# Optimization experiments

Measured on AMD Instinct MI355X. Metric: run time of the kernel, lower is better.

The kernel has to match this reference:

```python
import jax, jax.numpy as jnp
import numpy as np

B, S, D, H = 2, 2048, 1024, 16
HD = D // H  # head dim = 64


def setup_inputs() -> dict:
    key = jax.random.key(0)
    ks = jax.random.split(key, 9)
    s_in = 1.0 / np.sqrt(D)
    s_out = 1.0 / np.sqrt(HD)
    return {
        "x": jax.random.normal(ks[0], (B, S, D), jnp.float32),
        "Wq": jax.random.normal(ks[1], (D, H, HD), jnp.float32) * s_in,
        "bq": jnp.zeros((H, HD), jnp.float32),
        "Wk": jax.random.normal(ks[2], (D, H, HD), jnp.float32) * s_in,
        "bk": jnp.zeros((H, HD), jnp.float32),
        "Wv": jax.random.normal(ks[3], (D, H, HD), jnp.float32) * s_in,
        "bv": jnp.zeros((H, HD), jnp.float32),
        "Wo": jax.random.normal(ks[4], (H, HD, D), jnp.float32) * s_out,
        "bo": jnp.zeros((D,), jnp.float32),
    }


def reference(x, Wq, bq, Wk, bk, Wv, bv, Wo, bo):
    # QKV projections: [B,S,D] -> [B,S,H,HD]
    q = jnp.einsum("bsd,dhk->bshk", x, Wq) + bq
    k = jnp.einsum("bsd,dhk->bshk", x, Wk) + bk
    v = jnp.einsum("bsd,dhk->bshk", x, Wv) + bv

    # scaled dot-product attention (matches nnx.dot_product_attention)
    scale = jnp.asarray(1.0 / np.sqrt(HD), q.dtype)
    scores = jnp.einsum("bqhk,bshk->bhqs", q * scale, k)  # [B,H,S,S]
    attn = jax.nn.softmax(scores, axis=-1)
    y = jnp.einsum("bhqs,bshk->bqhk", attn, v)  # [B,S,H,HD]

    # exclusive post-processing: subtract projection onto L2-normalized v
    eps = jnp.asarray(1e-12, v.dtype)
    v_norm = v * jax.lax.rsqrt(jnp.sum(jnp.square(v), axis=-1, keepdims=True) + eps)
    y = y - jnp.sum(y * v_norm, axis=-1, keepdims=True) * v_norm

    # output projection: [B,S,H,HD] -> [B,S,D]
    out = jnp.einsum("bshk,hkd->bsd", y, Wo) + bo
    return out  # dropout is identity (deterministic=True)
```

## Files before the change

### kernel.cpp

```cpp
#include <hip/hip_runtime.h>

#define BB 2
#define SS 2048
#define DD 1024
#define HH 16
#define HDD 64

typedef __attribute__((ext_vector_type(4))) float f32x4;
typedef __attribute__((ext_vector_type(8))) short short8;
typedef __attribute__((ext_vector_type(4))) short short4v;

__device__ __forceinline__ short f2bf(float f) {
    union { float f; unsigned u; } a; a.f = f;
    unsigned r = a.u + 0x7fffu + ((a.u >> 16) & 1u);
    return (short)(r >> 16);
}
__device__ __forceinline__ float bf2f(short s) {
    union { unsigned u; float f; } a; a.u = ((unsigned)(unsigned short)s) << 16;
    return a.f;
}
__device__ __forceinline__ float fast_exp2(float x) {
    float r;
    asm("v_exp_f32 %0, %1\n\ts_nop 0" : "=v"(r) : "v"(x));
    return r;
}
__device__ __forceinline__ unsigned cvt_pk_bf16(float lo, float hi) {
    unsigned r;
    asm("v_cvt_pk_bf16_f32 %0, %1, %2" : "=v"(r) : "v"(lo), "v"(hi));
    return r;
}
__device__ __forceinline__ float fmax3(float a, float b, float c) {
    float r;
    asm("v_max3_f32 %0, %1, %2, %3" : "=v"(r) : "v"(a), "v"(b), "v"(c));
    return r;
}

#define GLD16(gp, lp) __builtin_amdgcn_global_load_lds( \
    (const __attribute__((address_space(1))) void*)(gp), \
    (__attribute__((address_space(3))) void*)(lp), 16, 0, 0)

__global__ __launch_bounds__(256) void conv_x(const float* __restrict__ src,
                                              short* __restrict__ dst)
{
    const int i = (blockIdx.x * 256 + threadIdx.x) * 8;
    f32x4 a = *(const f32x4*)(src + i);
    f32x4 b = *(const f32x4*)(src + i + 4);
    short8 o;
    #pragma unroll
    for (int j = 0; j < 4; j++) { o[j] = f2bf(a[j]); o[j + 4] = f2bf(b[j]); }
    *(short8*)(dst + i) = o;
}

__global__ __launch_bounds__(256) void conv_w4(
    const float* __restrict__ Wq, const float* __restrict__ Wk,
    const float* __restrict__ Wv, const float* __restrict__ Wo,
    short* __restrict__ Wt, short* __restrict__ Wot, float qscale)
{
    __shared__ float t[64][65];
    const int z = blockIdx.z;
    const float* src = (z == 0) ? Wq : (z == 1) ? Wk : (z == 2) ? Wv : Wo;
    short* dst = (z < 3) ? (Wt + (size_t)z * 1048576) : Wot;
    const float scale = (z == 0) ? qscale : 1.f;

    const int tid = threadIdx.x;
    const int c = tid & 63, rg = tid >> 6;
    const int bi = blockIdx.x * 64, bj = blockIdx.y * 64;
    #pragma unroll
    for (int i = 0; i < 16; i++)
        t[rg * 16 + i][c] = src[(size_t)(bi + rg * 16 + i) * 1024 + bj + c];
    __syncthreads();
    #pragma unroll
    for (int i = 0; i < 16; i++)
        dst[(size_t)(bj + rg * 16 + i) * 1024 + bi + c] = f2bf(scale * t[c][rg * 16 + i]);
}

__global__ __launch_bounds__(256) void conv_bias(const float* __restrict__ bq,
                                                 const float* __restrict__ bk,
                                                 const float* __restrict__ bv,
                                                 float* __restrict__ bcat, float qscale)
{
    const int i = blockIdx.x * 256 + threadIdx.x;
    float v = (i < 1024) ? bq[i] * qscale : (i < 2048 ? bk[i - 1024] : bv[i - 2048]);
    bcat[i] = v;
}

template<int KIND>
__global__ __launch_bounds__(256, 2) void gemm_mfma(
    const short* __restrict__ A, const short* __restrict__ Bt,
    const float* __restrict__ bias,
    short* __restrict__ oQ, short* __restrict__ oK, short* __restrict__ oV,
    float* __restrict__ oF)
{
    __shared__ short lds[32768];
    const int tid = threadIdx.x;
    const int lane = tid & 63;
    const int ln15 = lane & 15, g = lane >> 4;
    const int wid = tid >> 6;
    const int wm = wid >> 1, wn = wid & 1;
    const int bm = blockIdx.x * 128;
    const int bn = blockIdx.y * 128;
    const bool vpath = (KIND == 0) && (blockIdx.y >= 16);

    f32x4 acc[4][4];
    #pragma unroll
    for (int i = 0; i < 4; i++)
        #pragma unroll
        for (int j = 0; j < 4; j++) acc[i][j] = (f32x4){0.f, 0.f, 0.f, 0.f};

    const int sr = lane >> 3, cs = lane & 7;
    const int sc8 = (cs ^ sr) << 3;
    const int rb = wid * 8;

    auto stage = [&](int buf, int k0) {
        #pragma unroll
        for (int j = 0; j < 4; j++) {
            const int r = rb + j * 32 + sr;
            GLD16(A + (size_t)(bm + r) * 1024 + k0 + sc8,
                  &lds[buf * 16384 + (rb + j * 32) * 64]);
            GLD16(Bt + (size_t)(bn + r) * 1024 + k0 + sc8,
                  &lds[buf * 16384 + 8192 + (rb + j * 32) * 64]);
        }
    };

    stage(0, 0);
    asm volatile("s_waitcnt vmcnt(0)" ::: "memory");
    __builtin_amdgcn_s_barrier();

    for (int t = 0; t < 16; ++t) {
        const int cur = t & 1;
        if (t < 15) stage(cur ^ 1, (t + 1) * 64);
        const char* base = (const char*)lds + cur * 32768;

        #pragma unroll
        for (int kk = 0; kk < 2; kk++) {
            short8 af[4], bf[4];
            #pragma unroll
            for (int f = 0; f < 4; f++) {
                const int ra = wm * 64 + f * 16 + ln15;
                af[f] = *(const short8*)(base + ra * 128 +
                                         ((((kk << 2) | g) ^ (ra & 7)) << 4));
                const int rbv = wn * 64 + f * 16 + ln15;
                bf[f] = *(const short8*)(base + 16384 + rbv * 128 +
                                         ((((kk << 2) | g) ^ (rbv & 7)) << 4));
            }
            __builtin_amdgcn_s_setprio(1);
            if (!vpath) {
                #pragma unroll
                for (int fm = 0; fm < 4; fm++)
                    #pragma unroll
                    for (int fn = 0; fn < 4; fn++)
                        acc[fm][fn] = __builtin_amdgcn_mfma_f32_16x16x32_bf16(
                            bf[fn], af[fm], acc[fm][fn], 0, 0, 0);
            } else {
                #pragma unroll
                for (int fm = 0; fm < 4; fm++)
                    #pragma unroll
                    for (int fn = 0; fn < 4; fn++)
                        acc[fm][fn] = __builtin_amdgcn_mfma_f32_16x16x32_bf16(
                            af[fm], bf[fn], acc[fm][fn], 0, 0, 0);
            }
            __builtin_amdgcn_s_setprio(0);
        }
        asm volatile("s_waitcnt vmcnt(0) lgkmcnt(0)" ::: "memory");
        __builtin_amdgcn_s_barrier();
    }

    const int n_base = bn + wn * 64;

    if constexpr (KIND == 1) {
        #pragma unroll
        for (int fn = 0; fn < 4; fn++) {
            const int n0 = n_base + fn * 16 + 4 * g;
            const f32x4 b4 = *(const f32x4*)(bias + n0);
            #pragma unroll
            for (int fm = 0; fm < 4; fm++) {
                const int t = bm + wm * 64 + fm * 16 + ln15;
                f32x4 o = acc[fm][fn] + b4;
                *(f32x4*)(oF + (size_t)t * 1024 + n0) = o;
            }
        }
    } else if (!vpath) {
        short* dst = (n_base < 1024) ? oQ : oK;
        #pragma unroll
        for (int fn = 0; fn < 4; fn++) {
            const int n0 = n_base + fn * 16 + 4 * g;
            const f32x4 b4 = *(const f32x4*)(bias + n0);
            const int nl = n0 & 1023;
            const int h = nl >> 6, d = nl & 63;
            #pragma unroll
            for (int fm = 0; fm < 4; fm++) {
                const int t = bm + wm * 64 + fm * 16 + ln15;
                const int b = t >> 11, s = t & 2047;
                short4v pk = { f2bf(acc[fm][fn][0] + b4[0]), f2bf(acc[fm][fn][1] + b4[1]),
                               f2bf(acc[fm][fn][2] + b4[2]), f2bf(acc[fm][fn][3] + b4[3]) };
                *(short4v*)(dst + ((size_t)(b * HH + h) * SS + s) * HDD + d) = pk;
            }
        }
    } else {
        #pragma unroll
        for (int fn = 0; fn < 4; fn++) {
            const int nf = n_base + fn * 16 + ln15;
            const float bb = bias[nf];
            const int nl = nf - 2048;
            const int h = nl >> 6, d = nl & 63;
            #pragma unroll
            for (int fm = 0; fm < 4; fm++) {
                const int t0 = bm + wm * 64 + fm * 16 + 4 * g;
                const int b = t0 >> 11;
                const int sb = (t0 & 2047) & ~63;
                const int pos = g * 16 + (fm & 1) * 4 + ((fm >> 1) & 1) * 8;
                short4v pk = { f2bf(acc[fm][fn][0] + bb), f2bf(acc[fm][fn][1] + bb),
                               f2bf(acc[fm][fn][2] + bb), f2bf(acc[fm][fn][3] + bb) };
                *(short4v*)(oV + ((size_t)(b * HH + h) * HDD + d) * SS + sb + pos) = pk;
            }
        }
    }
}

__global__ __launch_bounds__(256, 2) void attn_mfma_kernel(
    const short* __restrict__ Qh, const short* __restrict__ Kh,
    const short* __restrict__ Vt, short* __restrict__ yb)
{
    __shared__ short lds[16384];

    const int lane = threadIdx.x & 63;
    const int wid  = threadIdx.x >> 6;
    const int ln15 = lane & 15;
    const int g    = lane >> 4;

    const int bid  = ((int)blockIdx.x & 7) * 64 + ((int)blockIdx.x >> 3);
    const int bh   = bid >> 4;
    const int qB   = (bid & 15) * 128;
    const int qW   = qB + wid * 32;

    const short* qbase = Qh + (size_t)bh * SS * HDD;
    const short* kbase = Kh + (size_t)bh * SS * HDD;
    const short* vtb   = Vt + (size_t)bh * HDD * SS;

    short8 qf[2][2];
    #pragma unroll
    for (int qg = 0; qg < 2; qg++)
        #pragma unroll
        for (int c = 0; c < 2; c++)
            qf[qg][c] = *(const short8*)(qbase +
                (size_t)(qW + qg * 16 + ln15) * HDD + c * 32 + g * 8);

    const short8 ones = { 0x3f80, 0x3f80, 0x3f80, 0x3f80,
                          0x3f80, 0x3f80, 0x3f80, 0x3f80 };

    const int sr = lane >> 3;
    const int cs = lane & 7;
    const int sc8 = (cs ^ sr) << 3;

    auto stage = [&](int b, int s0) {
        #pragma unroll
        for (int j = 0; j < 2; j++) {
            const int rr = wid * 16 + j * 8 + sr;
            GLD16(kbase + (size_t)(s0 + rr) * HDD + sc8,
                  &lds[b * 8192 + (wid * 16 + j * 8) * 64]);
            GLD16(vtb + (size_t)rr * SS + s0 + sc8,
                  &lds[b * 8192 + 4096 + (wid * 16 + j * 8) * 64]);
        }
    };

    f32x4 o[2][4], ol[2];
    #pragma unroll
    for (int qg = 0; qg < 2; qg++) {
        ol[qg] = (f32x4){0.f, 0.f, 0.f, 0.f};
        #pragma unroll
        for (int c = 0; c < 4; c++) o[qg][c] = (f32x4){0.f, 0.f, 0.f, 0.f};
    }
    float m[2] = { -1e30f, -1e30f };

    stage(0, 0);
    asm volatile("s_waitcnt vmcnt(0)" ::: "memory");
    __builtin_amdgcn_s_barrier();

    for (int t = 0; t < SS / 64; ++t) {
        const int cur = t & 1;
        if (t < SS / 64 - 1) stage(cur ^ 1, (t + 1) * 64);

        const char* kb = (const char*)lds + cur * 16384;
        short8 kf[4][2];
        #pragma unroll
        for (int kg = 0; kg < 4; kg++) {
            const int rk = kg * 16 + ln15;
            #pragma unroll
            for (int c = 0; c < 2; c++)
                kf[kg][c] = *(const short8*)(kb + rk * 128 +
                                             (((c * 4 + g) ^ (rk & 7)) << 4));
        }
        const f32x4 z = {0.f, 0.f, 0.f, 0.f};
        f32x4 s[4][2];
        __builtin_amdgcn_s_setprio(1);
        #pragma unroll
        for (int kg = 0; kg < 4; kg++)
            #pragma unroll
            for (int qg = 0; qg < 2; qg++) {
                s[kg][qg] = __builtin_amdgcn_mfma_f32_16x16x32_bf16(
                    kf[kg][0], qf[qg][0], z, 0, 0, 0);
                s[kg][qg] = __builtin_amdgcn_mfma_f32_16x16x32_bf16(
                    kf[kg][1], qf[qg][1], s[kg][qg], 0, 0, 0);
            }
        __builtin_amdgcn_s_setprio(0);

        float pm[2];
        #pragma unroll
        for (int qg = 0; qg < 2; qg++) {
            const float t0 = fmax3(s[0][qg][0], s[0][qg][1], s[0][qg][2]);
            const float t1 = fmax3(s[0][qg][3], s[1][qg][0], s[1][qg][1]);
            const float t2 = fmax3(s[1][qg][2], s[1][qg][3], s[2][qg][0]);
            const float t3 = fmax3(s[2][qg][1], s[2][qg][2], s[2][qg][3]);
            const float t4 = fmax3(s[3][qg][0], s[3][qg][1], s[3][qg][2]);
            pm[qg] = fmaxf(fmax3(t0, t1, t2), fmax3(t3, t4, s[3][qg][3]));
        }
        if (__any((pm[0] > m[0] + 8.f) || (pm[1] > m[1] + 8.f))) {
            #pragma unroll
            for (int qg = 0; qg < 2; qg++) {
                float pmw = fmaxf(pm[qg], __shfl_xor(pm[qg], 16));
                pmw = fmaxf(pmw, __shfl_xor(pmw, 32));
                const float mn = fmaxf(m[qg], pmw);
                const float corr = fast_exp2(m[qg] - mn);
                ol[qg] *= corr;
                #pragma unroll
                for (int c = 0; c < 4; c++) o[qg][c] *= corr;
                m[qg] = mn;
            }
        }

        union { unsigned u[4]; short8 v; } P0[2], P1[2];
        #pragma unroll
        for (int qg = 0; qg < 2; qg++) {
            float p[16];
            #pragma unroll
            for (int kg = 0; kg < 4; kg++)
                #pragma unroll
                for (int r = 0; r < 4; r++)
                    p[kg * 4 + r] = fast_exp2(s[kg][qg][r] - m[qg]);
            P0[qg].u[0] = cvt_pk_bf16(p[0], p[1]);
            P0[qg].u[1] = cvt_pk_bf16(p[2], p[3]);
            P0[qg].u[2] = cvt_pk_bf16(p[4], p[5]);
            P0[qg].u[3] = cvt_pk_bf16(p[6], p[7]);
            P1[qg].u[0] = cvt_pk_bf16(p[8], p[9]);
            P1[qg].u[1] = cvt_pk_bf16(p[10], p[11]);
            P1[qg].u[2] = cvt_pk_bf16(p[12], p[13]);
            P1[qg].u[3] = cvt_pk_bf16(p[14], p[15]);
        }

        const char* vb = kb + 8192;
        __builtin_amdgcn_s_setprio(1);
        #pragma unroll
        for (int c = 0; c < 4; c++) {
            const int rv = c * 16 + ln15;
            const int sw = ln15 & 7;
            short8 vf0 = *(const short8*)(vb + rv * 128 + (((2 * g) ^ sw) << 4));
            short8 vf1 = *(const short8*)(vb + rv * 128 + (((2 * g + 1) ^ sw) << 4));
            #pragma unroll
            for (int qg = 0; qg < 2; qg++) {
                o[qg][c] = __builtin_amdgcn_mfma_f32_16x16x32_bf16(
                    vf0, P0[qg].v, o[qg][c], 0, 0, 0);
                o[qg][c] = __builtin_amdgcn_mfma_f32_16x16x32_bf16(
                    vf1, P1[qg].v, o[qg][c], 0, 0, 0);
            }
        }
        #pragma unroll
        for (int qg = 0; qg < 2; qg++) {
            ol[qg] = __builtin_amdgcn_mfma_f32_16x16x32_bf16(ones, P0[qg].v, ol[qg], 0, 0, 0);
            ol[qg] = __builtin_amdgcn_mfma_f32_16x16x32_bf16(ones, P1[qg].v, ol[qg], 0, 0, 0);
        }
        __builtin_amdgcn_s_setprio(0);

        asm volatile("s_waitcnt vmcnt(0) lgkmcnt(0)" ::: "memory");
        __builtin_amdgcn_s_barrier();
    }

    const int b = bh >> 4, h = bh & 15;
    #pragma unroll
    for (int qg = 0; qg < 2; qg++) {
        const float inv = 1.f / ol[qg][0];
        #pragma unroll
        for (int c = 0; c < 4; c++) o[qg][c] *= inv;

        const int spos = qB + (wid >> 1) * 64 + (ln15 >> 2) * 16 + qg * 4 +
                         (wid & 1) * 8 + (ln15 & 3);
        float v4[4][4];
        float nv = 0.f, dv = 0.f;
        #pragma unroll
        for (int c = 0; c < 4; c++)
            #pragma unroll
            for (int r = 0; r < 4; r++) {
                const float vd = bf2f(vtb[(size_t)(c * 16 + 4 * g + r) * SS + spos]);
                v4[c][r] = vd;
                nv += vd * vd;
                dv += o[qg][c][r] * vd;
            }
        nv += __shfl_xor(nv, 16); nv += __shfl_xor(nv, 32);
        dv += __shfl_xor(dv, 16); dv += __shfl_xor(dv, 32);
        const float tpp = dv / (nv + 1e-12f);

        const int tok = b * SS + qW + qg * 16 + ln15;
        #pragma unroll
        for (int c = 0; c < 4; c++) {
            short4v pk = { f2bf(o[qg][c][0] - v4[c][0] * tpp),
                           f2bf(o[qg][c][1] - v4[c][1] * tpp),
                           f2bf(o[qg][c][2] - v4[c][2] * tpp),
                           f2bf(o[qg][c][3] - v4[c][3] * tpp) };
            *(short4v*)(yb + (size_t)tok * 1024 + h * 64 + c * 16 + 4 * g) = pk;
        }
    }
}

extern "C" void kernel_launch(void* const* d_in, const int* in_sizes, int n_in,
                              void* d_out, int out_size, void* d_ws, size_t ws_size,
                              hipStream_t stream)
{
    const float* x  = (const float*)d_in[0];
    const float* Wq = (const float*)d_in[1];
    const float* bq = (const float*)d_in[2];
    const float* Wk = (const float*)d_in[3];
    const float* bk = (const float*)d_in[4];
    const float* Wv = (const float*)d_in[5];
    const float* bv = (const float*)d_in[6];
    const float* Wo = (const float*)d_in[7];
    const float* bo = (const float*)d_in[8];
    float* out = (float*)d_out;

    char* w = (char*)d_ws;
    short* xb   = (short*)(w);
    short* Wt   = (short*)(w + (8ull << 20));
    short* Wot  = (short*)(w + (14ull << 20));
    float* bcat = (float*)(w + (16ull << 20));
    short* Qh   = (short*)(w + (17ull << 20));
    short* Kh   = (short*)(w + (25ull << 20));
    short* Vt   = (short*)(w + (33ull << 20));
    short* yb   = (short*)(w + (41ull << 20));

    const float qscale = 0.125f * 1.44269504f;
    dim3 blk(256);

    conv_x<<<2048, blk, 0, stream>>>(x, xb);
    conv_w4<<<dim3(16, 16, 4), blk, 0, stream>>>(Wq, Wk, Wv, Wo, Wt, Wot, qscale);
    conv_bias<<<12, blk, 0, stream>>>(bq, bk, bv, bcat, qscale);

    gemm_mfma<0><<<dim3(32, 24), blk, 0, stream>>>(xb, Wt, bcat,
                                                   Qh, Kh, Vt, nullptr);

    attn_mfma_kernel<<<dim3(512), blk, 0, stream>>>(Qh, Kh, Vt, yb);

    gemm_mfma<1><<<dim3(32, 8), blk, 0, stream>>>(yb, Wot, bo,
                                                  nullptr, nullptr, nullptr, out);
}
```

Baseline: 112.8 us.

## Merge conversion kernels, fold bias prep into GEMM, unroll double-buffered loops

The x conversion and the weight-transpose kernels are merged into one launch, and the bias-concatenation kernel is dropped so the QKV GEMM epilogue reads bq/bk/bv directly and applies the q scale itself. Both the GEMM and attention main loops are manually unrolled by two with fixed buffer indices and precomputed LDS and global offsets, which removes per-iteration address arithmetic. The setprio calls around the GEMM MFMAs are removed. Together these cut launch count and scalar/VALU overhead, at the cost of larger code and a changed workspace layout.

```diff
diff --git a/kernel.cpp b/kernel.cpp
--- a/kernel.cpp
+++ b/kernel.cpp
@@ -39,25 +39,30 @@
     (const __attribute__((address_space(1))) void*)(gp), \
     (__attribute__((address_space(3))) void*)(lp), 16, 0, 0)
 
-__global__ __launch_bounds__(256) void conv_x(const float* __restrict__ src,
-                                              short* __restrict__ dst)
-{
-    const int i = (blockIdx.x * 256 + threadIdx.x) * 8;
-    f32x4 a = *(const f32x4*)(src + i);
-    f32x4 b = *(const f32x4*)(src + i + 4);
-    short8 o;
-    #pragma unroll
-    for (int j = 0; j < 4; j++) { o[j] = f2bf(a[j]); o[j + 4] = f2bf(b[j]); }
-    *(short8*)(dst + i) = o;
-}
-
-__global__ __launch_bounds__(256) void conv_w4(
+__global__ __launch_bounds__(256) void conv_all(
+    const float* __restrict__ x,
     const float* __restrict__ Wq, const float* __restrict__ Wk,
     const float* __restrict__ Wv, const float* __restrict__ Wo,
-    short* __restrict__ Wt, short* __restrict__ Wot, float qscale)
+    short* __restrict__ xb, short* __restrict__ Wt, short* __restrict__ Wot,
+    float qscale)
 {
+    const int z = blockIdx.z;
+    if (z == 4) {
+        const int id = blockIdx.x * 16 + blockIdx.y;
+        const size_t base = (size_t)id * 16384 + threadIdx.x * 8;
+        #pragma unroll
+        for (int it = 0; it < 8; ++it) {
+            const size_t i = base + (size_t)it * 2048;
+            f32x4 a = *(const f32x4*)(x + i);
+            f32x4 b = *(const f32x4*)(x + i + 4);
+            short8 o;
+            #pragma unroll
+            for (int j = 0; j < 4; j++) { o[j] = f2bf(a[j]); o[j + 4] = f2bf(b[j]); }
+            *(short8*)(xb + i) = o;
+        }
+        return;
+    }
     __shared__ float t[64][65];
-    const int z = blockIdx.z;
     const float* src = (z == 0) ? Wq : (z == 1) ? Wk : (z == 2) ? Wv : Wo;
     short* dst = (z < 3) ? (Wt + (size_t)z * 1048576) : Wot;
     const float scale = (z == 0) ? qscale : 1.f;
@@ -74,20 +79,11 @@
         dst[(size_t)(bj + rg * 16 + i) * 1024 + bi + c] = f2bf(scale * t[c][rg * 16 + i]);
 }
 
-__global__ __launch_bounds__(256) void conv_bias(const float* __restrict__ bq,
-                                                 const float* __restrict__ bk,
-                                                 const float* __restrict__ bv,
-                                                 float* __restrict__ bcat, float qscale)
-{
-    const int i = blockIdx.x * 256 + threadIdx.x;
-    float v = (i < 1024) ? bq[i] * qscale : (i < 2048 ? bk[i - 1024] : bv[i - 2048]);
-    bcat[i] = v;
-}
-
 template<int KIND>
 __global__ __launch_bounds__(256, 2) void gemm_mfma(
     const short* __restrict__ A, const short* __restrict__ Bt,
-    const float* __restrict__ bias,
+    const float* __restrict__ b0, const float* __restrict__ b1,
+    const float* __restrict__ b2, float qscale,
     short* __restrict__ oQ, short* __restrict__ oK, short* __restrict__ oV,
     float* __restrict__ oF)
 {
@@ -95,6 +91,7 @@
     const int tid = threadIdx.x;
     const int lane = tid & 63;
     const int ln15 = lane & 15, g = lane >> 4;
+    const int swl = ln15 & 7;
     const int wid = tid >> 6;
     const int wm = wid >> 1, wn = wid & 1;
     const int bm = blockIdx.x * 128;
@@ -110,40 +107,42 @@
     const int sr = lane >> 3, cs = lane & 7;
     const int sc8 = (cs ^ sr) << 3;
     const int rb = wid * 8;
-
-    auto stage = [&](int buf, int k0) {
+    const short* Ak = A;
+    const short* Bk = Bt;
+    int aoff[4], boff[4], adst[4];
+    #pragma unroll
+    for (int j = 0; j < 4; j++) {
+        aoff[j] = (bm + rb + j * 32 + sr) * 1024 + sc8;
+        boff[j] = (bn + rb + j * 32 + sr) * 1024 + sc8;
+        adst[j] = (rb + j * 32) * 64;
+    }
+
+    auto stage = [&](int BUF) {
         #pragma unroll
         for (int j = 0; j < 4; j++) {
-            const int r = rb + j * 32 + sr;
-            GLD16(A + (size_t)(bm + r) * 1024 + k0 + sc8,
-                  &lds[buf * 16384 + (rb + j * 32) * 64]);
-            GLD16(Bt + (size_t)(bn + r) * 1024 + k0 + sc8,
-                  &lds[buf * 16384 + 8192 + (rb + j * 32) * 64]);
-        }
+            GLD16(Ak + aoff[j], &lds[BUF * 16384 + adst[j]]);
+            GLD16(Bk + boff[j], &lds[BUF * 16384 + 8192 + adst[j]]);
+        }
+        Ak += 64; Bk += 64;
     };
 
-    stage(0, 0);
-    asm volatile("s_waitcnt vmcnt(0)" ::: "memory");
-    __builtin_amdgcn_s_barrier();
-
-    for (int t = 0; t < 16; ++t) {
-        const int cur = t & 1;
-        if (t < 15) stage(cur ^ 1, (t + 1) * 64);
-        const char* base = (const char*)lds + cur * 32768;
-
+    const char* ldsc = (const char*)lds;
+    int aB[2], bB[2];
+    #pragma unroll
+    for (int kk = 0; kk < 2; kk++) {
+        aB[kk] = (wm * 64 + ln15) * 128 + ((((kk << 2) | g) ^ swl) << 4);
+        bB[kk] = 16384 + (wn * 64 + ln15) * 128 + ((((kk << 2) | g) ^ swl) << 4);
+    }
+
+    auto tilec = [&](int BUF) {
         #pragma unroll
         for (int kk = 0; kk < 2; kk++) {
             short8 af[4], bf[4];
             #pragma unroll
             for (int f = 0; f < 4; f++) {
-                const int ra = wm * 64 + f * 16 + ln15;
-                af[f] = *(const short8*)(base + ra * 128 +
-                                         ((((kk << 2) | g) ^ (ra & 7)) << 4));
-                const int rbv = wn * 64 + f * 16 + ln15;
-                bf[f] = *(const short8*)(base + 16384 + rbv * 128 +
-                                         ((((kk << 2) | g) ^ (rbv & 7)) << 4));
-            }
-            __builtin_amdgcn_s_setprio(1);
+                af[f] = *(const short8*)(ldsc + BUF * 32768 + aB[kk] + f * 2048);
+                bf[f] = *(const short8*)(ldsc + BUF * 32768 + bB[kk] + f * 2048);
+            }
             if (!vpath) {
                 #pragma unroll
                 for (int fm = 0; fm < 4; fm++)
@@ -159,11 +158,29 @@
                         acc[fm][fn] = __builtin_amdgcn_mfma_f32_16x16x32_bf16(
                             af[fm], bf[fn], acc[fm][fn], 0, 0, 0);
             }
-            __builtin_amdgcn_s_setprio(0);
-        }
+        }
+    };
+
+    stage(0);
+    asm volatile("s_waitcnt vmcnt(0)" ::: "memory");
+    __builtin_amdgcn_s_barrier();
+
+    #pragma unroll 1
+    for (int i = 0; i < 7; ++i) {
+        stage(1);
+        tilec(0);
         asm volatile("s_waitcnt vmcnt(0) lgkmcnt(0)" ::: "memory");
         __builtin_amdgcn_s_barrier();
-    }
+        stage(0);
+        tilec(1);
+        asm volatile("s_waitcnt vmcnt(0) lgkmcnt(0)" ::: "memory");
+        __builtin_amdgcn_s_barrier();
+    }
+    stage(1);
+    tilec(0);
+    asm volatile("s_waitcnt vmcnt(0) lgkmcnt(0)" ::: "memory");
+    __builtin_amdgcn_s_barrier();
+    tilec(1);
 
     const int n_base = bn + wn * 64;
 
@@ -171,7 +188,7 @@
         #pragma unroll
         for (int fn = 0; fn < 4; fn++) {
             const int n0 = n_base + fn * 16 + 4 * g;
-            const f32x4 b4 = *(const f32x4*)(bias + n0);
+            const f32x4 b4 = *(const f32x4*)(b0 + n0);
             #pragma unroll
             for (int fm = 0; fm < 4; fm++) {
                 const int t = bm + wm * 64 + fm * 16 + ln15;
@@ -180,12 +197,16 @@
             }
         }
     } else if (!vpath) {
-        short* dst = (n_base < 1024) ? oQ : oK;
+        const bool isq = (n_base < 1024);
+        short* dst = isq ? oQ : oK;
+        const float* bp = isq ? b0 : b1;
+        const float scl = isq ? qscale : 1.f;
         #pragma unroll
         for (int fn = 0; fn < 4; fn++) {
             const int n0 = n_base + fn * 16 + 4 * g;
-            const f32x4 b4 = *(const f32x4*)(bias + n0);
             const int nl = n0 & 1023;
+            f32x4 b4 = *(const f32x4*)(bp + nl);
+            b4 *= scl;
             const int h = nl >> 6, d = nl & 63;
             #pragma unroll
             for (int fm = 0; fm < 4; fm++) {
@@ -200,8 +221,8 @@
         #pragma unroll
         for (int fn = 0; fn < 4; fn++) {
             const int nf = n_base + fn * 16 + ln15;
-            const float bb = bias[nf];
             const int nl = nf - 2048;
+            const float bb = b2[nl];
             const int h = nl >> 6, d = nl & 63;
             #pragma unroll
             for (int fm = 0; fm < 4; fm++) {
@@ -227,6 +248,7 @@
     const int wid  = threadIdx.x >> 6;
     const int ln15 = lane & 15;
     const int g    = lane >> 4;
+    const int swl  = ln15 & 7;
 
     const int bid  = ((int)blockIdx.x & 7) * 64 + ((int)blockIdx.x >> 3);
     const int bh   = bid >> 4;
@@ -251,17 +273,27 @@
     const int sr = lane >> 3;
     const int cs = lane & 7;
     const int sc8 = (cs ^ sr) << 3;
-
-    auto stage = [&](int b, int s0) {
-        #pragma unroll
-        for (int j = 0; j < 2; j++) {
-            const int rr = wid * 16 + j * 8 + sr;
-            GLD16(kbase + (size_t)(s0 + rr) * HDD + sc8,
-                  &lds[b * 8192 + (wid * 16 + j * 8) * 64]);
-            GLD16(vtb + (size_t)rr * SS + s0 + sc8,
-                  &lds[b * 8192 + 4096 + (wid * 16 + j * 8) * 64]);
-        }
+    const int r0 = wid * 16 + sr;
+    const int r1 = wid * 16 + 8 + sr;
+    const short* Kk = kbase;
+    const short* Vk = vtb;
+    const int koff0 = r0 * 64 + sc8, koff1 = r1 * 64 + sc8;
+    const int voff0 = r0 * 2048 + sc8, voff1 = r1 * 2048 + sc8;
+    const int d0 = (wid * 16) * 64, d1 = (wid * 16 + 8) * 64;
+
+    auto stage = [&](int BUF) {
+        GLD16(Kk + koff0, &lds[BUF * 8192 + d0]);
+        GLD16(Kk + koff1, &lds[BUF * 8192 + d1]);
+        GLD16(Vk + voff0, &lds[BUF * 8192 + 4096 + d0]);
+        GLD16(Vk + voff1, &lds[BUF * 8192 + 4096 + d1]);
+        Kk += 4096; Vk += 64;
     };
+
+    const char* ldsc = (const char*)lds;
+    const int kA0 = ln15 * 128 + ((g ^ swl) << 4);
+    const int kA1 = ln15 * 128 + (((4 + g) ^ swl) << 4);
+    const int vA0 = 8192 + ln15 * 128 + (((2 * g) ^ swl) << 4);
+    const int vA1 = 8192 + ln15 * 128 + (((2 * g + 1) ^ swl) << 4);
 
     f32x4 o[2][4], ol[2];
     #pragma unroll
@@ -272,23 +304,12 @@
     }
     float m[2] = { -1e30f, -1e30f };
 
-    stage(0, 0);
-    asm volatile("s_waitcnt vmcnt(0)" ::: "memory");
-    __builtin_amdgcn_s_barrier();
-
-    for (int t = 0; t < SS / 64; ++t) {
-        const int cur = t & 1;
-        if (t < SS / 64 - 1) stage(cur ^ 1, (t + 1) * 64);
-
-        const char* kb = (const char*)lds + cur * 16384;
+    auto tilec = [&](int BUF) {
         short8 kf[4][2];
         #pragma unroll
         for (int kg = 0; kg < 4; kg++) {
-            const int rk = kg * 16 + ln15;
-            #pragma unroll
-            for (int c = 0; c < 2; c++)
-                kf[kg][c] = *(const short8*)(kb + rk * 128 +
-                                             (((c * 4 + g) ^ (rk & 7)) << 4));
+            kf[kg][0] = *(const short8*)(ldsc + BUF * 16384 + kA0 + kg * 2048);
+            kf[kg][1] = *(const short8*)(ldsc + BUF * 16384 + kA1 + kg * 2048);
         }
         const f32x4 z = {0.f, 0.f, 0.f, 0.f};
         f32x4 s[4][2];
@@ -347,14 +368,11 @@
             P1[qg].u[3] = cvt_pk_bf16(p[14], p[15]);
         }
 
-        const char* vb = kb + 8192;
         __builtin_amdgcn_s_setprio(1);
         #pragma unroll
         for (int c = 0; c < 4; c++) {
-            const int rv = c * 16 + ln15;
-            const int sw = ln15 & 7;
-            short8 vf0 = *(const short8*)(vb + rv * 128 + (((2 * g) ^ sw) << 4));
-            short8 vf1 = *(const short8*)(vb + rv * 128 + (((2 * g + 1) ^ sw) << 4));
+            short8 vf0 = *(const short8*)(ldsc + BUF * 16384 + vA0 + c * 2048);
+            short8 vf1 = *(const short8*)(ldsc + BUF * 16384 + vA1 + c * 2048);
             #pragma unroll
             for (int qg = 0; qg < 2; qg++) {
                 o[qg][c] = __builtin_amdgcn_mfma_f32_16x16x32_bf16(
@@ -369,10 +387,28 @@
             ol[qg] = __builtin_amdgcn_mfma_f32_16x16x32_bf16(ones, P1[qg].v, ol[qg], 0, 0, 0);
         }
         __builtin_amdgcn_s_setprio(0);
-
+    };
+
+    stage(0);
+    asm volatile("s_waitcnt vmcnt(0)" ::: "memory");
+    __builtin_amdgcn_s_barrier();
+
+    #pragma unroll 1
+    for (int i = 0; i < 15; ++i) {
+        stage(1);
+        tilec(0);
         asm volatile("s_waitcnt vmcnt(0) lgkmcnt(0)" ::: "memory");
         __builtin_amdgcn_s_barrier();
-    }
+        stage(0);
+        tilec(1);
+        asm volatile("s_waitcnt vmcnt(0) lgkmcnt(0)" ::: "memory");
+        __builtin_amdgcn_s_barrier();
+    }
+    stage(1);
+    tilec(0);
+    asm volatile("s_waitcnt vmcnt(0) lgkmcnt(0)" ::: "memory");
+    __builtin_amdgcn_s_barrier();
+    tilec(1);
 
     const int b = bh >> 4, h = bh & 15;
     #pragma unroll
@@ -429,24 +465,22 @@
     short* xb   = (short*)(w);
     short* Wt   = (short*)(w + (8ull << 20));
     short* Wot  = (short*)(w + (14ull << 20));
-    float* bcat = (float*)(w + (16ull << 20));
-    short* Qh   = (short*)(w + (17ull << 20));
-    short* Kh   = (short*)(w + (25ull << 20));
-    short* Vt   = (short*)(w + (33ull << 20));
-    short* yb   = (short*)(w + (41ull << 20));
+    short* Qh   = (short*)(w + (16ull << 20));
+    short* Kh   = (short*)(w + (24ull << 20));
+    short* Vt   = (short*)(w + (32ull << 20));
+    short* yb   = (short*)(w + (40ull << 20));
 
     const float qscale = 0.125f * 1.44269504f;
     dim3 blk(256);
 
-    conv_x<<<2048, blk, 0, stream>>>(x, xb);
-    conv_w4<<<dim3(16, 16, 4), blk, 0, stream>>>(Wq, Wk, Wv, Wo, Wt, Wot, qscale);
-    conv_bias<<<12, blk, 0, stream>>>(bq, bk, bv, bcat, qscale);
-
-    gemm_mfma<0><<<dim3(32, 24), blk, 0, stream>>>(xb, Wt, bcat,
+    conv_all<<<dim3(16, 16, 5), blk, 0, stream>>>(x, Wq, Wk, Wv, Wo,
+                                                  xb, Wt, Wot, qscale);
+
+    gemm_mfma<0><<<dim3(32, 24), blk, 0, stream>>>(xb, Wt, bq, bk, bv, qscale,
                                                    Qh, Kh, Vt, nullptr);
 
     attn_mfma_kernel<<<dim3(512), blk, 0, stream>>>(Qh, Kh, Vt, yb);
 
-    gemm_mfma<1><<<dim3(32, 8), blk, 0, stream>>>(yb, Wot, bo,
+    gemm_mfma<1><<<dim3(32, 8), blk, 0, stream>>>(yb, Wot, bo, nullptr, nullptr, 1.f,
                                                   nullptr, nullptr, nullptr, out);
 }
```

New measurement: 103.7 us. -8.1%, faster.
